# Kernel tuning notes

Hardware: AMD Instinct MI355X
Metric: run time of the kernel (lower is better)

The kernel has to match this reference:

```python
import jax, jax.numpy as jnp
import numpy as np

K = 7
PAD = K // 2
C = 24          # latent_dim
ITERS = 4


def conv2d(x, w, b):
    # x: (B, Cin, H, W), w: (Cout, Cin, kh, kw) -> (B, Cout, H, W), SAME padding
    y = jax.lax.conv_general_dilated(
        x, w, window_strides=(1, 1), padding='SAME',
        dimension_numbers=('NCHW', 'OIHW', 'NCHW'))
    return y + b[None, :, None, None]


def unfold(x, H, W):
    # F.unfold(x, K, padding=PAD).view(B, C, K*K, H, W)
    # ordering: for each channel, kernel offsets row-major (kh outer, kw inner)
    xp = jnp.pad(x, ((0, 0), (0, 0), (PAD, PAD), (PAD, PAD)))
    patches = jnp.stack(
        [xp[:, :, i:i + H, j:j + W] for i in range(K) for j in range(K)],
        axis=2)  # (B, C, K*K, H, W)
    return patches


def setup_inputs() -> dict:
    key = jax.random.key(0)
    ks = jax.random.split(key, 8)
    B, H, W = 2, 256, 256
    depth = jax.random.normal(ks[0], (B, 1, H, W), dtype=jnp.float32)
    texture = jax.random.normal(ks[1], (B, 3, H, W), dtype=jnp.float32)
    # depth_proj: Conv2d(1, C, 3, padding=1)
    w_dp = jax.random.normal(ks[2], (C, 1, 3, 3), dtype=jnp.float32) * 0.1
    b_dp = jax.random.normal(ks[3], (C,), dtype=jnp.float32) * 0.1
    # kernel_predictor: Conv2d(3, C*K*K, 3, padding=1) followed by softmax(dim=1)
    w_kp = jax.random.normal(ks[4], (C * K * K, 3, 3, 3), dtype=jnp.float32) * 0.1
    b_kp = jax.random.normal(ks[5], (C * K * K,), dtype=jnp.float32) * 0.1
    # to_depth: Conv2d(C, 1, 1)
    w_td = jax.random.normal(ks[6], (1, C, 1, 1), dtype=jnp.float32) * 0.1
    b_td = jax.random.normal(ks[7], (1,), dtype=jnp.float32) * 0.1
    return {'depth': depth, 'texture': texture,
            'w_dp': w_dp, 'b_dp': b_dp,
            'w_kp': w_kp, 'b_kp': b_kp,
            'w_td': w_td, 'b_td': b_td}


def reference(depth, texture, w_dp, b_dp, w_kp, b_kp, w_td, b_td):
    B, _, H, W = depth.shape
    depth_latent = conv2d(depth, w_dp, b_dp)                    # (B, C, H, W)
    logits = conv2d(texture, w_kp, b_kp)                        # (B, C*K*K, H, W)
    kernels = jax.nn.softmax(logits, axis=1)                    # softmax over full channel dim
    kernels = kernels.reshape(B, C, K * K, H, W)
    unfolded = unfold(depth_latent, H, W)                       # (B, C, K*K, H, W)
    for it in range(ITERS):
        diffused = jnp.sum(kernels * unfolded, axis=2)          # (B, C, H, W)
        if it < ITERS - 1:
            unfolded = unfold(diffused, H, W)
    fused_depth = conv2d(diffused, w_td, b_td)                  # (B, 1, H, W)
    return fused_depth
```

## Files before the change

kernel.cpp:

```cpp
#include <hip/hip_runtime.h>

#define BB   2
#define HH   256
#define WW   256
#define HWSZ (HH * WW)
#define CC   24
#define KSZ  7
#define KK   49
#define PADK 3
#define G    8
#define CPG  3
#define LSTR 24
#define LOG2E 1.44269504088896340736f

typedef __attribute__((ext_vector_type(8))) short short8;
typedef __attribute__((ext_vector_type(4))) float float4v;

__device__ __forceinline__ short f2bf(float x) {
  unsigned u = __builtin_bit_cast(unsigned, x);
  unsigned r = u + 0x7FFFu + ((u >> 16) & 1u);
  return (short)(r >> 16);
}
__device__ __forceinline__ float bf2f(short h) {
  unsigned u = ((unsigned)(unsigned short)h) << 16;
  return __builtin_bit_cast(float, u);
}

__global__ __launch_bounds__(64) void k_wsetup(
    const float* __restrict__ w_kp, const float* __restrict__ b_kp,
    short* __restrict__ wsW) {
  int blk = blockIdx.x;
  int s = blk & 1, mt = (blk >> 1) & 3, cg = blk >> 3;
  for (int idx = threadIdx.x; idx < 640; idx += 64) {
    int row = idx / 40, k = idx % 40;
    int kk = mt * 16 + row;
    float v = 0.f;
    if (kk < KK && k < 28)
      v = ((k < 27) ? w_kp[((size_t)cg * KK + kk) * 27 + k]
                    : b_kp[cg * KK + kk]) * LOG2E;
    short hi = f2bf(v);
    short h = (s == 0) ? hi : f2bf(v - bf2f(hi));
    wsW[(size_t)blk * 640 + idx] = h;
  }
}

__global__ __launch_bounds__(256) void k_bsetup(
    const float* __restrict__ tex, short* __restrict__ wsB) {
  __shared__ float lt[3 * 324];
  __shared__ int lltk[32];
  int b = blockIdx.z;
  int x0 = blockIdx.x * 16, y0 = blockIdx.y * 16;
  int tile = blockIdx.y * 16 + blockIdx.x;
  int tid = threadIdx.x, lane = tid & 63, wv = tid >> 6;
  int q = lane >> 4, col = lane & 15;

  if (tid < 32) {
    int k = tid, v;
    if (k < 27) v = (k / 9) * 324 + ((k % 9) / 3) * 18 + (k % 3);
    else if (k == 27) v = -1;
    else v = -2;
    lltk[k] = v;
  }
  for (int idx = tid; idx < 972; idx += 256) {
    int ci = idx / 324, r = idx % 324;
    int iy = r / 18, ix = r % 18;
    int yy = y0 + iy - 1, xx = x0 + ix - 1;
    bool ok = (yy >= 0 && yy < HH && xx >= 0 && xx < WW);
    lt[idx] = ok ? tex[((size_t)b * 3 + ci) * HWSZ + yy * WW + xx] : 0.f;
  }
  __syncthreads();

  int tko[8];
#pragma unroll
  for (int j = 0; j < 8; ++j) tko[j] = lltk[q * 8 + j];
  int4* w4 = (int4*)wsB;
#pragma unroll
  for (int nt = 0; nt < 4; ++nt) {
    short8 hi, lo;
#pragma unroll
    for (int j = 0; j < 8; ++j) {
      int o = tko[j];
      float v = (o == -1) ? 1.f
                          : ((o == -2) ? 0.f : lt[o + (wv * 4 + nt) * 18 + col]);
      short h = f2bf(v);
      hi[j] = h;
      lo[j] = f2bf(v - bf2f(h));
    }
    size_t base = ((((size_t)(b * 256 + tile) * 4 + wv) * 4 + nt) * 2);
    w4[(base + 0) * 64 + lane] = __builtin_bit_cast(int4, hi);
    w4[(base + 1) * 64 + lane] = __builtin_bit_cast(int4, lo);
  }
}

template <bool FIRST, bool FINAL>
__global__ __launch_bounds__(256, 6) void k_diffuse_m(
    const float* __restrict__ depth, const float* __restrict__ src,
    const float* __restrict__ invZ, const float* __restrict__ w_dp,
    const float* __restrict__ b_dp, const short* __restrict__ wsW,
    const short* __restrict__ wsB, float* __restrict__ dst,
    float* __restrict__ part, const float* __restrict__ w_td) {
  __shared__ float lsrc[CPG * 22 * LSTR];
  __shared__ float ldp[576];
  __shared__ int loffs[64];

  int b = blockIdx.z / G, g = blockIdx.z % G, c0 = g * CPG;
  int x0 = blockIdx.x * 16, y0 = blockIdx.y * 16;
  int tile = blockIdx.y * 16 + blockIdx.x;
  int tid = threadIdx.x, lane = tid & 63, wv = tid >> 6;
  int q = lane >> 4, col = lane & 15;

  if (tid < 64)
    loffs[tid] = (tid < KK) ? ((tid / 7) - 3) * LSTR + ((tid % 7) - 3) : 0;
  if (FIRST) {
    for (int idx = tid; idx < 576; idx += 256) {
      int iy = idx / 24, ix = idx % 24;
      int yy = y0 + iy - 4, xx = x0 + ix - 4;
      bool ok = (yy >= 0 && yy < HH && xx >= 0 && xx < WW);
      ldp[idx] = ok ? depth[(size_t)b * HWSZ + yy * WW + xx] : 0.f;
    }
  }
  __syncthreads();

  for (int idx = tid; idx < 484; idx += 256) {
    int iy = idx / 22, ix = idx % 22;
    int yy = y0 + iy - PADK, xx = x0 + ix - PADK;
    bool ok = (yy >= 0 && yy < HH && xx >= 0 && xx < WW);
    if (FIRST) {
#pragma unroll
      for (int c = 0; c < CPG; ++c) {
        float a = b_dp[c0 + c];
#pragma unroll
        for (int dy = 0; dy < 3; ++dy)
#pragma unroll
          for (int dx = 0; dx < 3; ++dx)
            a = fmaf(w_dp[(c0 + c) * 9 + dy * 3 + dx],
                     ldp[(iy + dy) * 24 + (ix + dx)], a);
        lsrc[c * 22 * LSTR + iy * LSTR + ix] = ok ? a : 0.f;
      }
    } else {
      float sc = ok ? invZ[b * HWSZ + yy * WW + xx] : 0.f;
#pragma unroll
      for (int c = 0; c < CPG; ++c)
        lsrc[c * 22 * LSTR + iy * LSTR + ix] =
            ok ? src[((size_t)b * CC + c0 + c) * HWSZ + yy * WW + xx] * sc : 0.f;
    }
  }
  __syncthreads();

  const int4* wB = (const int4*)wsB + ((size_t)(b * 256 + tile) * 4 + wv) * 512;

#pragma unroll 1
  for (int np = 0; np < 2; ++np) {
    short8 Bh[2], Bl[2];
#pragma unroll
    for (int t = 0; t < 2; ++t) {
      int nt = np * 2 + t;
      Bh[t] = __builtin_bit_cast(short8, wB[(nt * 2 + 0) * 64 + lane]);
      Bl[t] = __builtin_bit_cast(short8, wB[(nt * 2 + 1) * 64 + lane]);
    }
    int basep = (wv * 4 + np * 2 + 3) * LSTR + col + 3;
    float zacc[2] = {0.f, 0.f}, res[2] = {0.f, 0.f};
    float accc[2] = {0.f, 0.f};

    const short* wp = wsW + (size_t)g * 15360 + col * 40 + q * 8;
    short8 nAh = *(const short8*)wp;
    short8 nAl = *(const short8*)(wp + 640);
#pragma unroll 1
    for (int idx = 0; idx < 12; ++idx) {
      short8 Ah = nAh, Al = nAl;
      if (idx < 11) {
        wp += 1280;
        nAh = *(const short8*)wp;
        nAl = *(const short8*)(wp + 640);
      }
      int c = idx >> 2, mt = idx & 3;
      int cb = basep + c * 2112;
      const float* p0 = lsrc + cb + loffs[mt * 16 + q * 4 + 0];
      const float* p1 = lsrc + cb + loffs[mt * 16 + q * 4 + 1];
      const float* p2 = lsrc + cb + loffs[mt * 16 + q * 4 + 2];
      const float* p3 = lsrc + cb + loffs[mt * 16 + q * 4 + 3];
#pragma unroll
      for (int t = 0; t < 2; ++t) {
        float4v C = {0.f, 0.f, 0.f, 0.f};
        C = __builtin_amdgcn_mfma_f32_16x16x32_bf16(Ah, Bh[t], C, 0, 0, 0);
        C = __builtin_amdgcn_mfma_f32_16x16x32_bf16(Ah, Bl[t], C, 0, 0, 0);
        C = __builtin_amdgcn_mfma_f32_16x16x32_bf16(Al, Bh[t], C, 0, 0, 0);
        if (mt < 3) {
          float e0 = __builtin_amdgcn_exp2f(C[0]);
          float e1 = __builtin_amdgcn_exp2f(C[1]);
          float e2 = __builtin_amdgcn_exp2f(C[2]);
          float e3 = __builtin_amdgcn_exp2f(C[3]);
          if (FIRST) zacc[t] += (e0 + e1) + (e2 + e3);
          float a = accc[t];
          a = fmaf(e0, p0[t * LSTR], a);
          a = fmaf(e1, p1[t * LSTR], a);
          a = fmaf(e2, p2[t * LSTR], a);
          a = fmaf(e3, p3[t * LSTR], a);
          accc[t] = a;
        } else {
          float e = (q == 0) ? __builtin_amdgcn_exp2f(C[0]) : 0.f;
          if (FIRST) zacc[t] += e;
          accc[t] = fmaf(e, p0[t * LSTR], accc[t]);
        }
      }
      if (mt == 3) {
#pragma unroll
        for (int t = 0; t < 2; ++t) {
          float v = accc[t];
          v += __shfl_xor(v, 16, 64);
          v += __shfl_xor(v, 32, 64);
          if (FINAL) {
            res[t] = fmaf(w_td[c0 + c], v, res[t]);
          } else {
            int p = (y0 + wv * 4 + np * 2 + t) * WW + (x0 + col);
            if (lane < 16) dst[((size_t)b * CC + c0 + c) * HWSZ + p] = v;
          }
          accc[t] = 0.f;
        }
      }
    }
#pragma unroll
    for (int t = 0; t < 2; ++t) {
      int p = (y0 + wv * 4 + np * 2 + t) * WW + (x0 + col);
      if (FIRST) {
        float z = zacc[t];
        z += __shfl_xor(z, 16, 64);
        z += __shfl_xor(z, 32, 64);
        if (lane < 16) part[(size_t)g * BB * HWSZ + b * HWSZ + p] = z;
      }
      if (FINAL) {
        if (lane < 16) part[(size_t)g * BB * HWSZ + b * HWSZ + p] = res[t];
      }
    }
  }
}

__global__ __launch_bounds__(256) void k_zred(const float* __restrict__ zpart,
                                              float* __restrict__ invZ) {
  int t = blockIdx.x * 256 + threadIdx.x;
  float z = 0.f;
#pragma unroll
  for (int g = 0; g < G; ++g) z += zpart[(size_t)g * BB * HWSZ + t];
  invZ[t] = 1.f / z;
}

__global__ __launch_bounds__(256) void k_final(const float* __restrict__ respart,
                                               const float* __restrict__ invZ,
                                               const float* __restrict__ b_td,
                                               float* __restrict__ out) {
  int t = blockIdx.x * 256 + threadIdx.x;
  float r = 0.f;
#pragma unroll
  for (int g = 0; g < G; ++g) r += respart[(size_t)g * BB * HWSZ + t];
  out[t] = fmaf(r, invZ[t], b_td[0]);
}

extern "C" void kernel_launch(void* const* d_in, const int* in_sizes, int n_in,
                              void* d_out, int out_size, void* d_ws, size_t ws_size,
                              hipStream_t stream) {
  const float* depth = (const float*)d_in[0];
  const float* tex   = (const float*)d_in[1];
  const float* w_dp  = (const float*)d_in[2];
  const float* b_dp  = (const float*)d_in[3];
  const float* w_kp  = (const float*)d_in[4];
  const float* b_kp  = (const float*)d_in[5];
  const float* w_td  = (const float*)d_in[6];
  const float* b_td  = (const float*)d_in[7];
  float* out = (float*)d_out;

  char* ws = (char*)d_ws;
  const size_t buf_b = (size_t)BB * CC * HWSZ * 4;
  float* bufA = (float*)ws;
  float* bufB = (float*)(ws + buf_b);
  float* part = (float*)(ws + 2 * buf_b);
  float* invZ = (float*)(ws + 2 * buf_b + (size_t)G * BB * HWSZ * 4);
  short* wsW  = (short*)(ws + 2 * buf_b + (size_t)G * BB * HWSZ * 4 +
                         (size_t)BB * HWSZ * 4);
  short* wsB  = (short*)(ws + 2 * buf_b + (size_t)G * BB * HWSZ * 4 +
                         (size_t)BB * HWSZ * 4 + 192 * 640 * 2);

  k_wsetup<<<dim3(192), dim3(64), 0, stream>>>(w_kp, b_kp, wsW);
  k_bsetup<<<dim3(16, 16, BB), dim3(256), 0, stream>>>(tex, wsB);

  dim3 grid(WW / 16, HH / 16, BB * G), blk(256);
  dim3 grid1(BB * HWSZ / 256), blk1(256);

  k_diffuse_m<true, false><<<grid, blk, 0, stream>>>(
      depth, nullptr, nullptr, w_dp, b_dp, wsW, wsB, bufB, part, w_td);
  k_zred<<<grid1, blk1, 0, stream>>>(part, invZ);
  k_diffuse_m<false, false><<<grid, blk, 0, stream>>>(
      depth, bufB, invZ, w_dp, b_dp, wsW, wsB, bufA, part, w_td);
  k_diffuse_m<false, false><<<grid, blk, 0, stream>>>(
      depth, bufA, invZ, w_dp, b_dp, wsW, wsB, bufB, part, w_td);
  k_diffuse_m<false, true><<<grid, blk, 0, stream>>>(
      depth, bufB, invZ, w_dp, b_dp, wsW, wsB, nullptr, part, w_td);
  k_final<<<grid1, blk1, 0, stream>>>(part, invZ, b_td, out);
}
```

Measured before the change: 295.6 us.

## Merge setup kernels, interleave MFMA chains, replace final reduce with atomics

Merges the two weight/texture setup kernels into one launch. Interleaves the two independent MFMA accumulation chains and hoists the LDS loads ahead of them to hide MFMA latency. Removes the final reduction kernel: k_zred now initialises the output with the bias, and the last diffusion pass scales by invZ and atomically adds each group's contribution into the output. This saves one launch and a partial-buffer round trip, at the cost of 8-way atomic contention and a summation order that is no longer deterministic.

```diff
diff --git a/kernel.cpp b/kernel.cpp
--- a/kernel.cpp
+++ b/kernel.cpp
@@ -11,6 +11,7 @@
 #define G    8
 #define CPG  3
 #define LSTR 24
+#define CSTR (22 * LSTR)
 #define LOG2E 1.44269504088896340736f
 
 typedef __attribute__((ext_vector_type(8))) short short8;
@@ -26,31 +27,31 @@
   return __builtin_bit_cast(float, u);
 }
 
-__global__ __launch_bounds__(64) void k_wsetup(
+__global__ __launch_bounds__(256) void k_setup(
     const float* __restrict__ w_kp, const float* __restrict__ b_kp,
-    short* __restrict__ wsW) {
-  int blk = blockIdx.x;
-  int s = blk & 1, mt = (blk >> 1) & 3, cg = blk >> 3;
-  for (int idx = threadIdx.x; idx < 640; idx += 64) {
-    int row = idx / 40, k = idx % 40;
-    int kk = mt * 16 + row;
-    float v = 0.f;
-    if (kk < KK && k < 28)
-      v = ((k < 27) ? w_kp[((size_t)cg * KK + kk) * 27 + k]
-                    : b_kp[cg * KK + kk]) * LOG2E;
-    short hi = f2bf(v);
-    short h = (s == 0) ? hi : f2bf(v - bf2f(hi));
-    wsW[(size_t)blk * 640 + idx] = h;
-  }
-}
-
-__global__ __launch_bounds__(256) void k_bsetup(
-    const float* __restrict__ tex, short* __restrict__ wsB) {
+    const float* __restrict__ tex, short* __restrict__ wsW,
+    short* __restrict__ wsB) {
   __shared__ float lt[3 * 324];
   __shared__ int lltk[32];
-  int b = blockIdx.z;
-  int x0 = blockIdx.x * 16, y0 = blockIdx.y * 16;
-  int tile = blockIdx.y * 16 + blockIdx.x;
+  int blk = blockIdx.x;
+  if (blk < 192) {
+    int s = blk & 1, mt = (blk >> 1) & 3, cg = blk >> 3;
+    for (int idx = threadIdx.x; idx < 640; idx += 256) {
+      int row = idx / 40, k = idx % 40;
+      int kk = mt * 16 + row;
+      float v = 0.f;
+      if (kk < KK && k < 28)
+        v = ((k < 27) ? w_kp[((size_t)cg * KK + kk) * 27 + k]
+                      : b_kp[cg * KK + kk]) * LOG2E;
+      short hi = f2bf(v);
+      short h = (s == 0) ? hi : f2bf(v - bf2f(hi));
+      wsW[(size_t)blk * 640 + idx] = h;
+    }
+    return;
+  }
+  int tb = blk - 192;
+  int b = tb >> 8, tile = tb & 255;
+  int y0 = (tile >> 4) * 16, x0 = (tile & 15) * 16;
   int tid = threadIdx.x, lane = tid & 63, wv = tid >> 6;
   int q = lane >> 4, col = lane & 15;
 
@@ -98,8 +99,9 @@
     const float* __restrict__ invZ, const float* __restrict__ w_dp,
     const float* __restrict__ b_dp, const short* __restrict__ wsW,
     const short* __restrict__ wsB, float* __restrict__ dst,
-    float* __restrict__ part, const float* __restrict__ w_td) {
-  __shared__ float lsrc[CPG * 22 * LSTR];
+    float* __restrict__ part, const float* __restrict__ w_td,
+    float* __restrict__ outp) {
+  __shared__ float lsrc[CPG * CSTR];
   __shared__ float ldp[576];
   __shared__ int loffs[64];
 
@@ -135,13 +137,13 @@
           for (int dx = 0; dx < 3; ++dx)
             a = fmaf(w_dp[(c0 + c) * 9 + dy * 3 + dx],
                      ldp[(iy + dy) * 24 + (ix + dx)], a);
-        lsrc[c * 22 * LSTR + iy * LSTR + ix] = ok ? a : 0.f;
+        lsrc[c * CSTR + iy * LSTR + ix] = ok ? a : 0.f;
       }
     } else {
       float sc = ok ? invZ[b * HWSZ + yy * WW + xx] : 0.f;
 #pragma unroll
       for (int c = 0; c < CPG; ++c)
-        lsrc[c * 22 * LSTR + iy * LSTR + ix] =
+        lsrc[c * CSTR + iy * LSTR + ix] =
             ok ? src[((size_t)b * CC + c0 + c) * HWSZ + yy * WW + xx] * sc : 0.f;
     }
   }
@@ -151,13 +153,10 @@
 
 #pragma unroll 1
   for (int np = 0; np < 2; ++np) {
-    short8 Bh[2], Bl[2];
-#pragma unroll
-    for (int t = 0; t < 2; ++t) {
-      int nt = np * 2 + t;
-      Bh[t] = __builtin_bit_cast(short8, wB[(nt * 2 + 0) * 64 + lane]);
-      Bl[t] = __builtin_bit_cast(short8, wB[(nt * 2 + 1) * 64 + lane]);
-    }
+    short8 Bh0 = __builtin_bit_cast(short8, wB[(np * 4 + 0) * 64 + lane]);
+    short8 Bl0 = __builtin_bit_cast(short8, wB[(np * 4 + 1) * 64 + lane]);
+    short8 Bh1 = __builtin_bit_cast(short8, wB[(np * 4 + 2) * 64 + lane]);
+    short8 Bl1 = __builtin_bit_cast(short8, wB[(np * 4 + 3) * 64 + lane]);
     int basep = (wv * 4 + np * 2 + 3) * LSTR + col + 3;
     float zacc[2] = {0.f, 0.f}, res[2] = {0.f, 0.f};
     float accc[2] = {0.f, 0.f};
@@ -174,34 +173,48 @@
         nAl = *(const short8*)(wp + 640);
       }
       int c = idx >> 2, mt = idx & 3;
-      int cb = basep + c * 2112;
-      const float* p0 = lsrc + cb + loffs[mt * 16 + q * 4 + 0];
-      const float* p1 = lsrc + cb + loffs[mt * 16 + q * 4 + 1];
-      const float* p2 = lsrc + cb + loffs[mt * 16 + q * 4 + 2];
-      const float* p3 = lsrc + cb + loffs[mt * 16 + q * 4 + 3];
-#pragma unroll
-      for (int t = 0; t < 2; ++t) {
-        float4v C = {0.f, 0.f, 0.f, 0.f};
-        C = __builtin_amdgcn_mfma_f32_16x16x32_bf16(Ah, Bh[t], C, 0, 0, 0);
-        C = __builtin_amdgcn_mfma_f32_16x16x32_bf16(Ah, Bl[t], C, 0, 0, 0);
-        C = __builtin_amdgcn_mfma_f32_16x16x32_bf16(Al, Bh[t], C, 0, 0, 0);
-        if (mt < 3) {
-          float e0 = __builtin_amdgcn_exp2f(C[0]);
-          float e1 = __builtin_amdgcn_exp2f(C[1]);
-          float e2 = __builtin_amdgcn_exp2f(C[2]);
-          float e3 = __builtin_amdgcn_exp2f(C[3]);
-          if (FIRST) zacc[t] += (e0 + e1) + (e2 + e3);
-          float a = accc[t];
-          a = fmaf(e0, p0[t * LSTR], a);
-          a = fmaf(e1, p1[t * LSTR], a);
-          a = fmaf(e2, p2[t * LSTR], a);
-          a = fmaf(e3, p3[t * LSTR], a);
-          accc[t] = a;
-        } else {
-          float e = (q == 0) ? __builtin_amdgcn_exp2f(C[0]) : 0.f;
-          if (FIRST) zacc[t] += e;
-          accc[t] = fmaf(e, p0[t * LSTR], accc[t]);
+      int mtb = mt * 16 + q * 4;
+      const float* lsc = lsrc + c * CSTR + basep;
+      int o0 = loffs[mtb + 0], o1 = loffs[mtb + 1];
+      int o2 = loffs[mtb + 2], o3 = loffs[mtb + 3];
+      float t00 = lsc[o0], t01 = lsc[o0 + LSTR];
+      float t10 = lsc[o1], t11 = lsc[o1 + LSTR];
+      float t20 = lsc[o2], t21 = lsc[o2 + LSTR];
+      float t30 = lsc[o3], t31 = lsc[o3 + LSTR];
+
+      float4v C0 = {0.f, 0.f, 0.f, 0.f}, C1 = {0.f, 0.f, 0.f, 0.f};
+      C0 = __builtin_amdgcn_mfma_f32_16x16x32_bf16(Ah, Bh0, C0, 0, 0, 0);
+      C1 = __builtin_amdgcn_mfma_f32_16x16x32_bf16(Ah, Bh1, C1, 0, 0, 0);
+      C0 = __builtin_amdgcn_mfma_f32_16x16x32_bf16(Ah, Bl0, C0, 0, 0, 0);
+      C1 = __builtin_amdgcn_mfma_f32_16x16x32_bf16(Ah, Bl1, C1, 0, 0, 0);
+      C0 = __builtin_amdgcn_mfma_f32_16x16x32_bf16(Al, Bh0, C0, 0, 0, 0);
+      C1 = __builtin_amdgcn_mfma_f32_16x16x32_bf16(Al, Bh1, C1, 0, 0, 0);
+
+      if (mt < 3) {
+        float e00 = __builtin_amdgcn_exp2f(C0[0]);
+        float e01 = __builtin_amdgcn_exp2f(C0[1]);
+        float e02 = __builtin_amdgcn_exp2f(C0[2]);
+        float e03 = __builtin_amdgcn_exp2f(C0[3]);
+        float e10 = __builtin_amdgcn_exp2f(C1[0]);
+        float e11 = __builtin_amdgcn_exp2f(C1[1]);
+        float e12 = __builtin_amdgcn_exp2f(C1[2]);
+        float e13 = __builtin_amdgcn_exp2f(C1[3]);
+        if (FIRST) {
+          zacc[0] += (e00 + e01) + (e02 + e03);
+          zacc[1] += (e10 + e11) + (e12 + e13);
         }
+        float a0 = accc[0], a1 = accc[1];
+        a0 = fmaf(e00, t00, a0); a1 = fmaf(e10, t01, a1);
+        a0 = fmaf(e01, t10, a0); a1 = fmaf(e11, t11, a1);
+        a0 = fmaf(e02, t20, a0); a1 = fmaf(e12, t21, a1);
+        a0 = fmaf(e03, t30, a0); a1 = fmaf(e13, t31, a1);
+        accc[0] = a0; accc[1] = a1;
+      } else {
+        float e0 = (q == 0) ? __builtin_amdgcn_exp2f(C0[0]) : 0.f;
+        float e1 = (q == 0) ? __builtin_amdgcn_exp2f(C1[0]) : 0.f;
+        if (FIRST) { zacc[0] += e0; zacc[1] += e1; }
+        accc[0] = fmaf(e0, t00, accc[0]);
+        accc[1] = fmaf(e1, t01, accc[1]);
       }
       if (mt == 3) {
 #pragma unroll
@@ -229,30 +242,25 @@
         if (lane < 16) part[(size_t)g * BB * HWSZ + b * HWSZ + p] = z;
       }
       if (FINAL) {
-        if (lane < 16) part[(size_t)g * BB * HWSZ + b * HWSZ + p] = res[t];
+        if (lane < 16) {
+          float iz = invZ[b * HWSZ + p];
+          atomicAdd(&outp[(size_t)b * HWSZ + p], res[t] * iz);
+        }
       }
     }
   }
 }
 
 __global__ __launch_bounds__(256) void k_zred(const float* __restrict__ zpart,
-                                              float* __restrict__ invZ) {
+                                              float* __restrict__ invZ,
+                                              const float* __restrict__ b_td,
+                                              float* __restrict__ outp) {
   int t = blockIdx.x * 256 + threadIdx.x;
   float z = 0.f;
 #pragma unroll
   for (int g = 0; g < G; ++g) z += zpart[(size_t)g * BB * HWSZ + t];
   invZ[t] = 1.f / z;
-}
-
-__global__ __launch_bounds__(256) void k_final(const float* __restrict__ respart,
-                                               const float* __restrict__ invZ,
-                                               const float* __restrict__ b_td,
-                                               float* __restrict__ out) {
-  int t = blockIdx.x * 256 + threadIdx.x;
-  float r = 0.f;
-#pragma unroll
-  for (int g = 0; g < G; ++g) r += respart[(size_t)g * BB * HWSZ + t];
-  out[t] = fmaf(r, invZ[t], b_td[0]);
+  outp[t] = b_td[0];
 }
 
 extern "C" void kernel_launch(void* const* d_in, const int* in_sizes, int n_in,
@@ -279,20 +287,18 @@
   short* wsB  = (short*)(ws + 2 * buf_b + (size_t)G * BB * HWSZ * 4 +
                          (size_t)BB * HWSZ * 4 + 192 * 640 * 2);
 
-  k_wsetup<<<dim3(192), dim3(64), 0, stream>>>(w_kp, b_kp, wsW);
-  k_bsetup<<<dim3(16, 16, BB), dim3(256), 0, stream>>>(tex, wsB);
+  k_setup<<<dim3(192 + 512), dim3(256), 0, stream>>>(w_kp, b_kp, tex, wsW, wsB);
 
   dim3 grid(WW / 16, HH / 16, BB * G), blk(256);
   dim3 grid1(BB * HWSZ / 256), blk1(256);
 
   k_diffuse_m<true, false><<<grid, blk, 0, stream>>>(
-      depth, nullptr, nullptr, w_dp, b_dp, wsW, wsB, bufB, part, w_td);
-  k_zred<<<grid1, blk1, 0, stream>>>(part, invZ);
+      depth, nullptr, nullptr, w_dp, b_dp, wsW, wsB, bufB, part, w_td, nullptr);
+  k_zred<<<grid1, blk1, 0, stream>>>(part, invZ, b_td, out);
   k_diffuse_m<false, false><<<grid, blk, 0, stream>>>(
-      depth, bufB, invZ, w_dp, b_dp, wsW, wsB, bufA, part, w_td);
+      depth, bufB, invZ, w_dp, b_dp, wsW, wsB, bufA, part, w_td, nullptr);
   k_diffuse_m<false, false><<<grid, blk, 0, stream>>>(
-      depth, bufA, invZ, w_dp, b_dp, wsW, wsB, bufB, part, w_td);
+      depth, bufA, invZ, w_dp, b_dp, wsW, wsB, bufB, part, w_td, nullptr);
   k_diffuse_m<false, true><<<grid, blk, 0, stream>>>(
-      depth, bufB, invZ, w_dp, b_dp, wsW, wsB, nullptr, part, w_td);
-  k_final<<<grid1, blk1, 0, stream>>>(part, invZ, b_td, out);
-}
+      depth, bufB, invZ, w_dp, b_dp, wsW, wsB, nullptr, part, w_td, out);
+}
```

New measurement: 296.1 us. Within noise of the previous version (+0.2%).
